# Kernel optimization log

Hardware: AMD Instinct MI355X
Metric: run time of the kernel (lower is better)

The kernel has to match this reference:

```python
import jax, jax.numpy as jnp
import numpy as np

WIRES = 4
KS = 2
STRIDE = 2
OUT_CH = 4
LAYERS = 4
N_ROT = 8
SEED = 42
RATIO_IMPRIM = 0.3  # pennylane RandomLayers default


def _build_structure():
    # Mimics pennylane.templates.RandomLayers with a fixed seed: per layer, draw
    # random single-qubit rotations (RX/RY/RZ on random wires, consuming weights)
    # interleaved with random CNOTs at ratio_imprim.
    rng = np.random.RandomState(SEED)
    gates = []
    for l in range(LAYERS):
        i = 0
        while i < N_ROT:
            if rng.random_sample() > RATIO_IMPRIM:
                g = int(rng.randint(3))  # 0:RX 1:RY 2:RZ
                w = int(rng.randint(WIRES))
                gates.append(("R", g, w, l, i))
                i += 1
            else:
                cw, tw = rng.choice(WIRES, 2, replace=False)
                gates.append(("CNOT", int(cw), int(tw), 0, 0))
    return gates

GATES = _build_structure()


def _apply_1q(state, U, wire):
    # state: [P,2,2,2,2]; U: [2,2] shared or [P,2,2] per-patch
    ax = wire + 1
    s = jnp.moveaxis(state, ax, -1)
    if U.ndim == 2:
        s = jnp.einsum('ab,...b->...a', U, s)
    else:
        s = jnp.einsum('pab,p...b->p...a', U, s)
    return jnp.moveaxis(s, -1, ax)


def _apply_cnot(state, control, target):
    c_ax, t_ax = control + 1, target + 1
    s0 = jax.lax.index_in_dim(state, 0, c_ax, keepdims=False)
    s1 = jax.lax.index_in_dim(state, 1, c_ax, keepdims=False)
    t2 = t_ax - 1 if t_ax > c_ax else t_ax  # target axis after removing control axis
    return jnp.stack([s0, jnp.flip(s1, axis=t2)], axis=c_ax)


def _rot(g, t):
    h = t * 0.5
    c = jnp.cos(h)
    s = jnp.sin(h)
    z = jnp.zeros_like(c)
    if g == 0:    # RX
        U = jnp.stack([jnp.stack([c + 0j, -1j * s]), jnp.stack([-1j * s, c + 0j])])
    elif g == 1:  # RY
        U = jnp.stack([jnp.stack([c + 0j, -s + 0j]), jnp.stack([s + 0j, c + 0j])])
    else:         # RZ
        U = jnp.stack([jnp.stack([c - 1j * s, z + 0j]), jnp.stack([z + 0j, c + 1j * s])])
    return U.astype(jnp.complex64)


def _circuit(angles, weights):
    # angles: [P,4] RY encoding angles; returns [P, OUT_CH] PauliZ expvals
    P = angles.shape[0]
    state = jnp.zeros((P,) + (2,) * WIRES, jnp.complex64)
    state = state.at[(slice(None),) + (0,) * WIRES].set(1.0)
    for j in range(KS * KS):  # data-encoding RY, per-patch angle
        h = angles[:, j] * 0.5
        c, s = jnp.cos(h), jnp.sin(h)
        U = jnp.stack([jnp.stack([c, -s], -1), jnp.stack([s, c], -1)], -2).astype(jnp.complex64)
        state = _apply_1q(state, U, j)
    for kind, a, b, l, i in GATES:
        if kind == "R":
            state = _apply_1q(state, _rot(a, weights[l, i]), b)
        else:
            state = _apply_cnot(state, a, b)
    probs = (state.real ** 2 + state.imag ** 2).reshape(P, 2 ** WIRES)
    idx = np.arange(2 ** WIRES)
    signs = np.stack([1.0 - 2.0 * ((idx >> (WIRES - 1 - j)) & 1) for j in range(OUT_CH)])
    return probs @ jnp.asarray(signs, jnp.float32).T


def setup_inputs() -> dict:
    key = jax.random.key(0)
    k1, k2 = jax.random.split(key)
    img = jax.random.uniform(k1, (32, 512, 512, 3), dtype=jnp.float32)
    weights = jax.random.uniform(k2, (LAYERS, N_ROT), dtype=jnp.float32) * (2.0 * np.pi)
    return {"img": img, "weights": weights}


def reference(img, weights):
    bs, h, w, ch = img.shape
    x = img.mean(axis=-1) if ch > 1 else img[..., 0]  # [bs,h,w]
    h_out = (h - KS) // STRIDE + 1
    w_out = (w - KS) // STRIDE + 1
    # Faithful to original loop: patches only at j,k in range(0, h_out, stride),
    # written to out[j//kernel_size, k//kernel_size]; remaining entries stay zero.
    js = np.arange(0, h_out, STRIDE)
    ks_ = np.arange(0, w_out, STRIDE)
    ridx = js[:, None] + np.arange(KS)   # [nj,KS]
    cidx = ks_[:, None] + np.arange(KS)  # [nk,KS]
    patches = x[:, ridx]                 # [bs,nj,KS,w]
    patches = patches[:, :, :, cidx]     # [bs,nj,KS,nk,KS]
    patches = jnp.transpose(patches, (0, 1, 3, 2, 4)).reshape(-1, KS * KS)  # row-major like p.reshape(-1)
    res = _circuit(patches, weights)     # [P, OUT_CH]
    nj, nk = len(js), len(ks_)
    res = res.reshape(bs, nj, nk, OUT_CH).astype(jnp.float32)
    out = jnp.zeros((bs, h_out, w_out, OUT_CH), jnp.float32)
    out = out.at[:, js // KS[..., None] if False else (js // KS)[:, None], (ks_ // KS)[None, :], :].set(res)
    return out
```

## Files before the change

kernel.cpp:

```cpp
#include <hip/hip_runtime.h>
#include <cstdint>
#include <cstddef>

#define MAXG 128

namespace ct {

struct MT19937 {
  uint32_t mt[624] = {};
  int mti = 0;
  constexpr void seed(uint32_t s) {
    mt[0] = s;
    for (int i = 1; i < 624; i++)
      mt[i] = 1812433253u * (mt[i-1] ^ (mt[i-1] >> 30)) + (uint32_t)i;
    mti = 624;
  }
  constexpr uint32_t next() {
    if (mti >= 624) {
      for (int i = 0; i < 624; i++) {
        uint32_t y = (mt[i] & 0x80000000u) | (mt[(i+1) % 624] & 0x7fffffffu);
        mt[i] = mt[(i+397) % 624] ^ (y >> 1) ^ ((y & 1u) ? 2567483615u : 0u);
      }
      mti = 0;
    }
    uint32_t y = mt[mti++];
    y ^= y >> 11; y ^= (y << 7) & 2636928640u; y ^= (y << 15) & 4022730752u; y ^= y >> 18;
    return y;
  }
  constexpr double rdouble() {
    uint32_t a = next() >> 5, b = next() >> 6;
    return ((double)a * 67108864.0 + (double)b) / 9007199254740992.0;
  }
  constexpr uint32_t masked32(uint32_t rng, uint32_t mask) {
    uint32_t v = next() & mask;
    while (v > rng) v = next() & mask;
    return v;
  }
  constexpr uint32_t interval(uint32_t mx) {
    if (!mx) return 0;
    uint32_t mask = mx;
    mask |= mask >> 1; mask |= mask >> 2; mask |= mask >> 4; mask |= mask >> 8; mask |= mask >> 16;
    uint32_t v = next() & mask;
    while (v > mx) v = next() & mask;
    return v;
  }
};

struct CG { int n = 0; int code[MAXG] = {}; };

constexpr CG build_gates_ct() {
  CG gl{};
  MT19937 rng{};
  rng.seed(42);
  for (int l = 0; l < 4; l++) {
    int i = 0;
    while (i < 8) {
      if (rng.rdouble() > 0.3) {
        int g = (int)rng.masked32(2, 3);
        int w = (int)rng.masked32(3, 3);
        int widx = l * 8 + i;
        if (gl.n < MAXG) gl.code[gl.n++] = g | ((8 >> w) << 2) | (widx << 6);
        i++;
      } else {
        int perm[4] = {0, 1, 2, 3};
        for (int ii = 3; ii >= 1; ii--) {
          int j = (int)rng.interval((uint32_t)ii);
          int tmp = perm[ii]; perm[ii] = perm[j]; perm[j] = tmp;
        }
        int cw = perm[0], tw = perm[1];
        if (gl.n < MAXG) gl.code[gl.n++] = 3 | ((8 >> cw) << 2) | ((8 >> tw) << 6);
      }
    }
  }
  return gl;
}

constexpr CG GL = build_gates_ct();

}

typedef __attribute__((ext_vector_type(8))) short short8;
typedef __attribute__((ext_vector_type(4))) float f32x4;

__device__ __forceinline__ void half_sincos(float a, float& s, float& c) {
  const float r = a * 0.07957747154594767f;
  s = __builtin_amdgcn_sinf(r);
  c = __builtin_amdgcn_cosf(r);
}

__device__ __forceinline__ float hi_part(float a) {
  return __uint_as_float(__float_as_uint(a) & 0xffff0000u);
}
__device__ __forceinline__ unsigned pack_hi(float a, float b) {
  return (__float_as_uint(a) >> 16) | (__float_as_uint(b) & 0xffff0000u);
}
__device__ __forceinline__ short8 pack8(float v0, float v1, float v2, float v3,
                                        float v4, float v5, float v6, float v7) {
  union { unsigned u[4]; short8 s; } r;
  r.u[0] = pack_hi(v0, v1); r.u[1] = pack_hi(v2, v3);
  r.u[2] = pack_hi(v4, v5); r.u[3] = pack_hi(v6, v7);
  return r.s;
}

template <int G>
__device__ __forceinline__ void apply_gates(float (&sr)[16], float (&si)[16],
                                            const float* __restrict__ w) {
  if constexpr (G < ct::GL.n) {
    constexpr int code = ct::GL.code[G];
    constexpr int kind = code & 3;
    if constexpr (kind == 3) {
      constexpr int cbit = (code >> 2) & 15, tbit = (code >> 6) & 15;
      float tr[16], ti[16];
      #pragma unroll
      for (int k = 0; k < 16; k++) {
        const int src = (k & cbit) ? (k ^ tbit) : k;
        tr[k] = sr[src]; ti[k] = si[src];
      }
      #pragma unroll
      for (int k = 0; k < 16; k++) { sr[k] = tr[k]; si[k] = ti[k]; }
    } else {
      constexpr int bit  = (code >> 2) & 15;
      constexpr int widx = (code >> 6) & 31;
      float sh, ch;
      half_sincos(w[widx], sh, ch);
      float tr[16], ti[16];
      #pragma unroll
      for (int k = 0; k < 16; k++) {
        const int p = k ^ bit;
        if constexpr (kind == 0) {
          tr[k] = ch * sr[k] + sh * si[p];
          ti[k] = ch * si[k] - sh * sr[p];
        } else if constexpr (kind == 1) {
          if (k & bit) { tr[k] = ch * sr[k] + sh * sr[p]; ti[k] = ch * si[k] + sh * si[p]; }
          else         { tr[k] = ch * sr[k] - sh * sr[p]; ti[k] = ch * si[k] - sh * si[p]; }
        } else {
          if (k & bit) { tr[k] = ch * sr[k] - sh * si[k]; ti[k] = ch * si[k] + sh * sr[k]; }
          else         { tr[k] = ch * sr[k] + sh * si[k]; ti[k] = ch * si[k] - sh * sr[k]; }
        }
      }
      #pragma unroll
      for (int k = 0; k < 16; k++) { sr[k] = tr[k]; si[k] = ti[k]; }
    }
    apply_gates<G + 1>(sr, si, w);
  }
}

__global__ __launch_bounds__(64) void build_u(const float* __restrict__ w,
                                              float* __restrict__ ws) {
  __shared__ float2 Ul[256];
  const int l = threadIdx.x;
  const int c = l & 15;
  float sr[16], si[16];
  #pragma unroll
  for (int k = 0; k < 16; k++) { sr[k] = (k == c) ? 1.0f : 0.0f; si[k] = 0.0f; }
  apply_gates<0>(sr, si, w);
  if (l < 16) {
    #pragma unroll
    for (int k = 0; k < 16; k++) Ul[k * 16 + c] = make_float2(sr[k], si[k]);
  }
  __syncthreads();

  const int row = l & 15, g = l >> 4;
  float re1[8], re2[8], im1[8], im2[8];
  #pragma unroll
  for (int j = 0; j < 8; j++) {
    const int kk = 8 * g + j;
    const int i = kk & 15;
    float2 u = Ul[row * 16 + i];
    float reh = hi_part(u.x), rel = u.x - reh;
    float imh = hi_part(u.y), iml = u.y - imh;
    re1[j] = reh;
    im1[j] = imh;
    re2[j] = (kk < 16) ? rel : 0.f;
    im2[j] = (kk < 16) ? iml : 0.f;
  }
  short8* o = (short8*)ws;
  o[l]       = pack8(re1[0],re1[1],re1[2],re1[3],re1[4],re1[5],re1[6],re1[7]);
  o[64 + l]  = pack8(re2[0],re2[1],re2[2],re2[3],re2[4],re2[5],re2[6],re2[7]);
  o[128 + l] = pack8(im1[0],im1[1],im1[2],im1[3],im1[4],im1[5],im1[6],im1[7]);
  o[192 + l] = pack8(im2[0],im2[1],im2[2],im2[3],im2[4],im2[5],im2[6],im2[7]);
}

__device__ __forceinline__ float4 tile_epi(const f32x4& ar, const f32x4& ai, int g) {
  float pk0 = ar[0]*ar[0] + ai[0]*ai[0];
  float pk1 = ar[1]*ar[1] + ai[1]*ai[1];
  float pk2 = ar[2]*ar[2] + ai[2]*ai[2];
  float pk3 = ar[3]*ar[3] + ai[3]*ai[3];
  float s  = (pk0 + pk1) + (pk2 + pk3);
  float p0 = (g & 2) ? -s : s;
  float p1 = (g & 1) ? -s : s;
  float p2 = (pk0 + pk1) - (pk2 + pk3);
  float p3 = (pk0 - pk1) + (pk2 - pk3);
  p0 += __shfl_xor(p0, 16); p0 += __shfl_xor(p0, 32);
  p1 += __shfl_xor(p1, 16); p1 += __shfl_xor(p1, 32);
  p2 += __shfl_xor(p2, 16); p2 += __shfl_xor(p2, 32);
  p3 += __shfl_xor(p3, 16); p3 += __shfl_xor(p3, 32);
  return make_float4(p0, p1, p2, p3);
}

__global__ __launch_bounds__(256) void qonv_mfma(const float* __restrict__ img,
                                                 const float* __restrict__ uws,
                                                 float* __restrict__ out) {
  __shared__ short slds[4][2048];
  const int t = threadIdx.x;
  const int lane = t & 63, w = t >> 6;
  const int c16 = lane & 15, g = lane >> 4;

  const short8* A8 = (const short8*)uws;
  const short8 Ar1 = A8[lane], Ar2 = A8[64 + lane];
  const short8 Ai1 = A8[128 + lane], Ai2 = A8[192 + lane];

  const unsigned W = blockIdx.x * 4u + (unsigned)w;
  const int b = W >> 8, jj = (W >> 1) & 127, kkb = (W & 1) * 64;
  const int kk = kkb + lane;

  {
    const unsigned PERB = 49152u;
    float4* o4 = (float4*)out;
    const float4 z = make_float4(0.f, 0.f, 0.f, 0.f);
    unsigned tid = blockIdx.x * 256u + (unsigned)t;
    #pragma unroll
    for (int it = 0; it < 3; it++) {
      unsigned zi = tid + (unsigned)it * 524288u;
      unsigned bb = zi / PERB;
      unsigned r = zi - bb * PERB;
      unsigned row, col;
      if (r < 16384u) { row = r >> 7;               col = 128u + (r & 127u); }
      else            { unsigned r2 = r - 16384u;   row = 128u + (r2 >> 8); col = r2 & 255u; }
      o4[((size_t)bb * 256u + row) * 256u + col] = z;
    }
  }

  const float* row0 = img + (size_t)(b * 512 + 2 * jj) * 1536 + 6 * kk;
  const float* row1 = row0 + 1536;
  const float inv3 = 1.0f / 3.0f;
  float2 x0 = *(const float2*)(row0);
  float2 x1 = *(const float2*)(row0 + 2);
  float2 x2 = *(const float2*)(row0 + 4);
  float2 y0 = *(const float2*)(row1);
  float2 y1 = *(const float2*)(row1 + 2);
  float2 y2 = *(const float2*)(row1 + 4);
  float a0 = (x0.x + x0.y + x1.x) * inv3;
  float a1 = (x1.y + x2.x + x2.y) * inv3;
  float a2 = (y0.x + y0.y + y1.x) * inv3;
  float a3 = (y1.y + y2.x + y2.y) * inv3;
  float c0, s0, c1, s1, c2, s2, c3, s3;
  half_sincos(a0, s0, c0);
  half_sincos(a1, s1, c1);
  half_sincos(a2, s2, c2);
  half_sincos(a3, s3, c3);
  float A4[4] = {c0 * c1, c0 * s1, s0 * c1, s0 * s1};
  float B4[4] = {c2 * c3, c2 * s3, s2 * c3, s2 * s3};
  float s16[16];
  #pragma unroll
  for (int hi = 0; hi < 4; hi++)
    #pragma unroll
    for (int lo = 0; lo < 4; lo++)
      s16[hi * 4 + lo] = A4[hi] * B4[lo];

  float sh_[16], sl_[16];
  #pragma unroll
  for (int i = 0; i < 16; i++) {
    float hv = hi_part(s16[i]);
    sh_[i] = hv; sl_[i] = s16[i] - hv;
  }

  short* wb = &slds[w][0];
  *(short8*)(wb + lane * 32 +  0) = pack8(sh_[0],sh_[1],sh_[2],sh_[3],sh_[4],sh_[5],sh_[6],sh_[7]);
  *(short8*)(wb + lane * 32 +  8) = pack8(sh_[8],sh_[9],sh_[10],sh_[11],sh_[12],sh_[13],sh_[14],sh_[15]);
  *(short8*)(wb + lane * 32 + 16) = pack8(sl_[0],sl_[1],sl_[2],sl_[3],sl_[4],sl_[5],sl_[6],sl_[7]);
  *(short8*)(wb + lane * 32 + 24) = pack8(sl_[8],sl_[9],sl_[10],sl_[11],sl_[12],sl_[13],sl_[14],sl_[15]);

  f32x4 zf = {0.f, 0.f, 0.f, 0.f};
  float4 res0, res1, res2, res3;
  {
    short8 B = *(const short8*)(wb + (0 * 16 + c16) * 32 + 8 * g);
    f32x4 ar = zf, ai = zf;
    ar = __builtin_amdgcn_mfma_f32_16x16x32_bf16(Ar1, B, ar, 0, 0, 0);
    ar = __builtin_amdgcn_mfma_f32_16x16x32_bf16(Ar2, B, ar, 0, 0, 0);
    ai = __builtin_amdgcn_mfma_f32_16x16x32_bf16(Ai1, B, ai, 0, 0, 0);
    ai = __builtin_amdgcn_mfma_f32_16x16x32_bf16(Ai2, B, ai, 0, 0, 0);
    res0 = tile_epi(ar, ai, g);
  }
  {
    short8 B = *(const short8*)(wb + (1 * 16 + c16) * 32 + 8 * g);
    f32x4 ar = zf, ai = zf;
    ar = __builtin_amdgcn_mfma_f32_16x16x32_bf16(Ar1, B, ar, 0, 0, 0);
    ar = __builtin_amdgcn_mfma_f32_16x16x32_bf16(Ar2, B, ar, 0, 0, 0);
    ai = __builtin_amdgcn_mfma_f32_16x16x32_bf16(Ai1, B, ai, 0, 0, 0);
    ai = __builtin_amdgcn_mfma_f32_16x16x32_bf16(Ai2, B, ai, 0, 0, 0);
    res1 = tile_epi(ar, ai, g);
  }
  {
    short8 B = *(const short8*)(wb + (2 * 16 + c16) * 32 + 8 * g);
    f32x4 ar = zf, ai = zf;
    ar = __builtin_amdgcn_mfma_f32_16x16x32_bf16(Ar1, B, ar, 0, 0, 0);
    ar = __builtin_amdgcn_mfma_f32_16x16x32_bf16(Ar2, B, ar, 0, 0, 0);
    ai = __builtin_amdgcn_mfma_f32_16x16x32_bf16(Ai1, B, ai, 0, 0, 0);
    ai = __builtin_amdgcn_mfma_f32_16x16x32_bf16(Ai2, B, ai, 0, 0, 0);
    res2 = tile_epi(ar, ai, g);
  }
  {
    short8 B = *(const short8*)(wb + (3 * 16 + c16) * 32 + 8 * g);
    f32x4 ar = zf, ai = zf;
    ar = __builtin_amdgcn_mfma_f32_16x16x32_bf16(Ar1, B, ar, 0, 0, 0);
    ar = __builtin_amdgcn_mfma_f32_16x16x32_bf16(Ar2, B, ar, 0, 0, 0);
    ai = __builtin_amdgcn_mfma_f32_16x16x32_bf16(Ai1, B, ai, 0, 0, 0);
    ai = __builtin_amdgcn_mfma_f32_16x16x32_bf16(Ai2, B, ai, 0, 0, 0);
    res3 = tile_epi(ar, ai, g);
  }

  float4 rA = (g & 1) ? res1 : res0;
  float4 rB = (g & 1) ? res3 : res2;
  float4 mine = (g & 2) ? rB : rA;
  ((float4*)out)[((size_t)b * 256 + jj) * 256 + kkb + lane] = mine;
}

extern "C" void kernel_launch(void* const* d_in, const int* in_sizes, int n_in,
                              void* d_out, int out_size, void* d_ws, size_t ws_size,
                              hipStream_t stream) {
  const float* img = (const float*)d_in[0];
  const float* wts = (const float*)d_in[1];
  float* out = (float*)d_out;

  build_u<<<1, 64, 0, stream>>>(wts, (float*)d_ws);
  qonv_mfma<<<2048, 256, 0, stream>>>(img, (const float*)d_ws, out);
}
```

Baseline: 21.01 us.

## Fuse unitary construction into main kernel and drop the build_u launch

Removes the separate single-block build_u launch and has 16 threads of every block rebuild the 16x16 circuit unitary into padded shared memory, then pack the bf16 hi/lo A fragments locally after a block barrier. The goal is to remove one kernel launch and the serialized dependency on a tiny one-block kernel. It also reorganizes the LDS staging layout so B-fragment reads are contiguous per lane group, and simplifies the zero-fill index math by replacing division with shifts. The cost is redundant gate evaluation in every block and a __syncthreads that stalls the other waves while 16 threads compute the unitary.

```diff
diff --git a/kernel.cpp b/kernel.cpp
--- a/kernel.cpp
+++ b/kernel.cpp
@@ -145,42 +145,6 @@
   }
 }
 
-__global__ __launch_bounds__(64) void build_u(const float* __restrict__ w,
-                                              float* __restrict__ ws) {
-  __shared__ float2 Ul[256];
-  const int l = threadIdx.x;
-  const int c = l & 15;
-  float sr[16], si[16];
-  #pragma unroll
-  for (int k = 0; k < 16; k++) { sr[k] = (k == c) ? 1.0f : 0.0f; si[k] = 0.0f; }
-  apply_gates<0>(sr, si, w);
-  if (l < 16) {
-    #pragma unroll
-    for (int k = 0; k < 16; k++) Ul[k * 16 + c] = make_float2(sr[k], si[k]);
-  }
-  __syncthreads();
-
-  const int row = l & 15, g = l >> 4;
-  float re1[8], re2[8], im1[8], im2[8];
-  #pragma unroll
-  for (int j = 0; j < 8; j++) {
-    const int kk = 8 * g + j;
-    const int i = kk & 15;
-    float2 u = Ul[row * 16 + i];
-    float reh = hi_part(u.x), rel = u.x - reh;
-    float imh = hi_part(u.y), iml = u.y - imh;
-    re1[j] = reh;
-    im1[j] = imh;
-    re2[j] = (kk < 16) ? rel : 0.f;
-    im2[j] = (kk < 16) ? iml : 0.f;
-  }
-  short8* o = (short8*)ws;
-  o[l]       = pack8(re1[0],re1[1],re1[2],re1[3],re1[4],re1[5],re1[6],re1[7]);
-  o[64 + l]  = pack8(re2[0],re2[1],re2[2],re2[3],re2[4],re2[5],re2[6],re2[7]);
-  o[128 + l] = pack8(im1[0],im1[1],im1[2],im1[3],im1[4],im1[5],im1[6],im1[7]);
-  o[192 + l] = pack8(im2[0],im2[1],im2[2],im2[3],im2[4],im2[5],im2[6],im2[7]);
-}
-
 __device__ __forceinline__ float4 tile_epi(const f32x4& ar, const f32x4& ai, int g) {
   float pk0 = ar[0]*ar[0] + ai[0]*ai[0];
   float pk1 = ar[1]*ar[1] + ai[1]*ai[1];
@@ -198,36 +162,42 @@
   return make_float4(p0, p1, p2, p3);
 }
 
-__global__ __launch_bounds__(256) void qonv_mfma(const float* __restrict__ img,
-                                                 const float* __restrict__ uws,
-                                                 float* __restrict__ out) {
-  __shared__ short slds[4][2048];
+__global__ __launch_bounds__(256) void qonv_fused(const float* __restrict__ img,
+                                                  const float* __restrict__ wts,
+                                                  float* __restrict__ out) {
+  __shared__ short stage[4][4][64][8];
+  __shared__ float2 Uws[512];
   const int t = threadIdx.x;
   const int lane = t & 63, w = t >> 6;
   const int c16 = lane & 15, g = lane >> 4;
 
-  const short8* A8 = (const short8*)uws;
-  const short8 Ar1 = A8[lane], Ar2 = A8[64 + lane];
-  const short8 Ai1 = A8[128 + lane], Ai2 = A8[192 + lane];
+  if (t < 16) {
+    const int c = t;
+    float sr[16], si[16];
+    #pragma unroll
+    for (int k = 0; k < 16; k++) { sr[k] = (k == c) ? 1.0f : 0.0f; si[k] = 0.0f; }
+    apply_gates<0>(sr, si, wts);
+    #pragma unroll
+    for (int k = 0; k < 16; k++) Uws[k * 17 + c] = make_float2(sr[k], si[k]);
+  }
 
   const unsigned W = blockIdx.x * 4u + (unsigned)w;
   const int b = W >> 8, jj = (W >> 1) & 127, kkb = (W & 1) * 64;
   const int kk = kkb + lane;
 
   {
-    const unsigned PERB = 49152u;
     float4* o4 = (float4*)out;
     const float4 z = make_float4(0.f, 0.f, 0.f, 0.f);
-    unsigned tid = blockIdx.x * 256u + (unsigned)t;
+    const unsigned tid = blockIdx.x * 256u + (unsigned)t;
+    {
+      unsigned bb = tid >> 14, rr = tid & 16383u;
+      o4[((size_t)bb * 256u + (rr >> 7)) * 256u + 128u + (rr & 127u)] = z;
+    }
     #pragma unroll
-    for (int it = 0; it < 3; it++) {
+    for (int it = 0; it < 2; it++) {
       unsigned zi = tid + (unsigned)it * 524288u;
-      unsigned bb = zi / PERB;
-      unsigned r = zi - bb * PERB;
-      unsigned row, col;
-      if (r < 16384u) { row = r >> 7;               col = 128u + (r & 127u); }
-      else            { unsigned r2 = r - 16384u;   row = 128u + (r2 >> 8); col = r2 & 255u; }
-      o4[((size_t)bb * 256u + row) * 256u + col] = z;
+      unsigned bb = zi >> 15, rr = zi & 32767u;
+      o4[((size_t)bb * 256u + 128u + (rr >> 8)) * 256u + (rr & 255u)] = z;
     }
   }
 
@@ -265,16 +235,31 @@
     sh_[i] = hv; sl_[i] = s16[i] - hv;
   }
 
-  short* wb = &slds[w][0];
-  *(short8*)(wb + lane * 32 +  0) = pack8(sh_[0],sh_[1],sh_[2],sh_[3],sh_[4],sh_[5],sh_[6],sh_[7]);
-  *(short8*)(wb + lane * 32 +  8) = pack8(sh_[8],sh_[9],sh_[10],sh_[11],sh_[12],sh_[13],sh_[14],sh_[15]);
-  *(short8*)(wb + lane * 32 + 16) = pack8(sl_[0],sl_[1],sl_[2],sl_[3],sl_[4],sl_[5],sl_[6],sl_[7]);
-  *(short8*)(wb + lane * 32 + 24) = pack8(sl_[8],sl_[9],sl_[10],sl_[11],sl_[12],sl_[13],sl_[14],sl_[15]);
+  *(short8*)&stage[w][0][lane][0] = pack8(sh_[0],sh_[1],sh_[2],sh_[3],sh_[4],sh_[5],sh_[6],sh_[7]);
+  *(short8*)&stage[w][1][lane][0] = pack8(sh_[8],sh_[9],sh_[10],sh_[11],sh_[12],sh_[13],sh_[14],sh_[15]);
+  *(short8*)&stage[w][2][lane][0] = pack8(sl_[0],sl_[1],sl_[2],sl_[3],sl_[4],sl_[5],sl_[6],sl_[7]);
+  *(short8*)&stage[w][3][lane][0] = pack8(sl_[8],sl_[9],sl_[10],sl_[11],sl_[12],sl_[13],sl_[14],sl_[15]);
+
+  __syncthreads();
+
+  float re1[8], re2[8], im1[8], im2[8];
+  #pragma unroll
+  for (int j = 0; j < 8; j++) {
+    float2 u = Uws[c16 * 17 + (g & 1) * 8 + j];
+    float reh = hi_part(u.x), imh = hi_part(u.y);
+    re1[j] = reh; im1[j] = imh;
+    re2[j] = (g < 2) ? (u.x - reh) : 0.f;
+    im2[j] = (g < 2) ? (u.y - imh) : 0.f;
+  }
+  const short8 Ar1 = pack8(re1[0],re1[1],re1[2],re1[3],re1[4],re1[5],re1[6],re1[7]);
+  const short8 Ar2 = pack8(re2[0],re2[1],re2[2],re2[3],re2[4],re2[5],re2[6],re2[7]);
+  const short8 Ai1 = pack8(im1[0],im1[1],im1[2],im1[3],im1[4],im1[5],im1[6],im1[7]);
+  const short8 Ai2 = pack8(im2[0],im2[1],im2[2],im2[3],im2[4],im2[5],im2[6],im2[7]);
 
   f32x4 zf = {0.f, 0.f, 0.f, 0.f};
   float4 res0, res1, res2, res3;
   {
-    short8 B = *(const short8*)(wb + (0 * 16 + c16) * 32 + 8 * g);
+    short8 B = *(const short8*)&stage[w][g][0 * 16 + c16][0];
     f32x4 ar = zf, ai = zf;
     ar = __builtin_amdgcn_mfma_f32_16x16x32_bf16(Ar1, B, ar, 0, 0, 0);
     ar = __builtin_amdgcn_mfma_f32_16x16x32_bf16(Ar2, B, ar, 0, 0, 0);
@@ -283,7 +268,7 @@
     res0 = tile_epi(ar, ai, g);
   }
   {
-    short8 B = *(const short8*)(wb + (1 * 16 + c16) * 32 + 8 * g);
+    short8 B = *(const short8*)&stage[w][g][1 * 16 + c16][0];
     f32x4 ar = zf, ai = zf;
     ar = __builtin_amdgcn_mfma_f32_16x16x32_bf16(Ar1, B, ar, 0, 0, 0);
     ar = __builtin_amdgcn_mfma_f32_16x16x32_bf16(Ar2, B, ar, 0, 0, 0);
@@ -292,7 +277,7 @@
     res1 = tile_epi(ar, ai, g);
   }
   {
-    short8 B = *(const short8*)(wb + (2 * 16 + c16) * 32 + 8 * g);
+    short8 B = *(const short8*)&stage[w][g][2 * 16 + c16][0];
     f32x4 ar = zf, ai = zf;
     ar = __builtin_amdgcn_mfma_f32_16x16x32_bf16(Ar1, B, ar, 0, 0, 0);
     ar = __builtin_amdgcn_mfma_f32_16x16x32_bf16(Ar2, B, ar, 0, 0, 0);
@@ -301,7 +286,7 @@
     res2 = tile_epi(ar, ai, g);
   }
   {
-    short8 B = *(const short8*)(wb + (3 * 16 + c16) * 32 + 8 * g);
+    short8 B = *(const short8*)&stage[w][g][3 * 16 + c16][0];
     f32x4 ar = zf, ai = zf;
     ar = __builtin_amdgcn_mfma_f32_16x16x32_bf16(Ar1, B, ar, 0, 0, 0);
     ar = __builtin_amdgcn_mfma_f32_16x16x32_bf16(Ar2, B, ar, 0, 0, 0);
@@ -323,6 +308,5 @@
   const float* wts = (const float*)d_in[1];
   float* out = (float*)d_out;
 
-  build_u<<<1, 64, 0, stream>>>(wts, (float*)d_ws);
-  qonv_mfma<<<2048, 256, 0, stream>>>(img, (const float*)d_ws, out);
-}
+  qonv_fused<<<2048, 256, 0, stream>>>(img, wts, out);
+}
```

Result: slower. 23.86 us (+13.5%).
